# Performance work log

Measured on AMD Instinct MI355X. Metric: run time of the kernel, lower is better.

## Reference

```python
import jax, jax.numpy as jnp
import numpy as np

B, H, S, D = 4, 16, 2048, 64

def setup_inputs() -> dict:
    key = jax.random.key(0)
    kq, kk, kv = jax.random.split(key, 3)
    return {
        "query": jax.random.normal(kq, (B, H, S, D), dtype=jnp.float32),
        "key": jax.random.normal(kk, (B, H, S, D), dtype=jnp.float32),
        "value": jax.random.normal(kv, (B, H, S, D), dtype=jnp.float32),
        "dropout_p": 0,
    }

def reference(query, key, value, dropout_p):
    # qk: [B,H,S,S] materialized as in the original (unfused SDPA)
    scale = query.shape[-1] ** -0.5
    qk = jnp.einsum("bhqd,bhkd->bhqk", query, key) * scale
    attn = jax.nn.softmax(qk, axis=-1)
    # dropout_p == 0 -> identity (keeps reference deterministic)
    out = jnp.einsum("bhqk,bhkd->bhqd", attn, value)
    return out
```

## Files before the change

### kernel.cpp

```cpp
#include <hip/hip_runtime.h>
#include <hip/hip_bf16.h>

#define B_   4
#define H_   16
#define SEQ  2048
#define DH   64
#define BM   128
#define BN   128
#define NBH  (B_ * H_)
#define NELEM (NBH * SEQ * DH)

typedef __bf16 bf16x8 __attribute__((ext_vector_type(8)));
typedef float  f32x4  __attribute__((ext_vector_type(4)));
typedef unsigned short u16x8 __attribute__((ext_vector_type(8)));
typedef unsigned short u16x4 __attribute__((ext_vector_type(4)));

__device__ __forceinline__ unsigned short f2bu(float x) {
    __hip_bfloat16 h = __float2bfloat16(x);
    return __builtin_bit_cast(unsigned short, h);
}

__device__ __forceinline__ void ld_lds16(const unsigned short* g, unsigned short* l) {
    __builtin_amdgcn_global_load_lds(
        (const __attribute__((address_space(1))) unsigned int*)(g),
        (__attribute__((address_space(3))) unsigned int*)(l), 16, 0, 0);
}

__global__ __launch_bounds__(256)
void prep_kv(const float* __restrict__ K, const float* __restrict__ V,
             unsigned short* __restrict__ Kb, unsigned short* __restrict__ Vt) {
    __shared__ unsigned short tile[64 * 72];
    const int bh = blockIdx.y;
    const int s0 = blockIdx.x * 64;
    const int t  = threadIdx.x;

    {
        const float* Ki = K + (size_t)bh * SEQ * DH + (size_t)s0 * DH;
        unsigned short* Ko = Kb + (size_t)bh * SEQ * DH + (size_t)s0 * DH;
        for (int j = 0; j < 4; ++j) {
            const int e = (j * 256 + t) * 4;
            const float4 v = *reinterpret_cast<const float4*>(Ki + e);
            u16x4 u; u[0] = f2bu(v.x); u[1] = f2bu(v.y); u[2] = f2bu(v.z); u[3] = f2bu(v.w);
            *reinterpret_cast<u16x4*>(Ko + e) = u;
        }
    }

    const float* Vb = V + (size_t)bh * SEQ * DH + (size_t)s0 * DH;
    unsigned short* Vo = Vt + (size_t)bh * DH * SEQ;
    {
        const int sl = t >> 2, d0 = (t & 3) * 16;
        for (int c = 0; c < 4; ++c) {
            const float4 v = *reinterpret_cast<const float4*>(Vb + sl * DH + d0 + c * 4);
            u16x4 u; u[0] = f2bu(v.x); u[1] = f2bu(v.y); u[2] = f2bu(v.z); u[3] = f2bu(v.w);
            *reinterpret_cast<u16x4*>(&tile[sl * 72 + d0 + c * 4]) = u;
        }
    }
    __syncthreads();
    {
        const int d = t >> 2, sc = (t & 3) * 16;
        for (int j = 0; j < 4; ++j) {
            u16x4 u;
            u[0] = tile[(sc + 4 * j + 0) * 72 + d];
            u[1] = tile[(sc + 4 * j + 1) * 72 + d];
            u[2] = tile[(sc + 4 * j + 2) * 72 + d];
            u[3] = tile[(sc + 4 * j + 3) * 72 + d];
            *reinterpret_cast<u16x4*>(Vo + (size_t)d * SEQ + s0 + sc + 4 * j) = u;
        }
    }
}

__global__ __launch_bounds__(256, 3)
void fa_fwd(const float* __restrict__ Qg, const unsigned short* __restrict__ Kb,
            const unsigned short* __restrict__ Vtb, float* __restrict__ Og)
{
    __shared__ __attribute__((aligned(16))) unsigned short smem[16384];
    unsigned short* Klds = smem;
    unsigned short* Vlds = smem + 8192;

    const int tid  = threadIdx.x;
    const int lane = tid & 63;
    const int wave = tid >> 6;
    const int l15  = lane & 15;
    const int quad = lane >> 4;

    const int qtile = blockIdx.x;
    const int bh    = blockIdx.y;

    const float*          Qb  = Qg  + (size_t)bh * SEQ * DH;
    const unsigned short* Kbh = Kb  + (size_t)bh * SEQ * DH;
    const unsigned short* Vbh = Vtb + (size_t)bh * DH * SEQ;
    float*                Ob  = Og  + (size_t)bh * SEQ * DH;

    const int qrow0 = qtile * BM + wave * 32;

    const float CS = 0.125f * 1.4426950408889634f;

    bf16x8 Qf[2][2];
    for (int rt = 0; rt < 2; ++rt) {
        const float* qsrc = Qb + (size_t)(qrow0 + rt * 16 + l15) * DH + quad * 8;
        for (int kt = 0; kt < 2; ++kt) {
            const float4 a = *reinterpret_cast<const float4*>(qsrc + kt * 32);
            const float4 b = *reinterpret_cast<const float4*>(qsrc + kt * 32 + 4);
            union { bf16x8 v; unsigned short u[8]; } tmp;
            tmp.u[0] = f2bu(a.x * CS); tmp.u[1] = f2bu(a.y * CS);
            tmp.u[2] = f2bu(a.z * CS); tmp.u[3] = f2bu(a.w * CS);
            tmp.u[4] = f2bu(b.x * CS); tmp.u[5] = f2bu(b.y * CS);
            tmp.u[6] = f2bu(b.z * CS); tmp.u[7] = f2bu(b.w * CS);
            Qf[rt][kt] = tmp.v;
        }
    }

    bf16x8 ones;
    {
        union { bf16x8 v; unsigned short u[8]; } t;
        for (int i = 0; i < 8; ++i) t.u[i] = 0x3F80;
        ones = t.v;
    }
    const f32x4 fzero = {0.f, 0.f, 0.f, 0.f};

    f32x4 Oacc[2][4];
    f32x4 Lacc[2];
    for (int rt = 0; rt < 2; ++rt) {
        Lacc[rt] = fzero;
        for (int dt = 0; dt < 4; ++dt) Oacc[rt][dt] = fzero;
    }

    const unsigned short* kp[4];
    const unsigned short* vp[4];
    unsigned short* klp[4];
    unsigned short* vlp[4];
    for (int i = 0; i < 4; ++i) {
        const int beta = i * 256 + tid;
        {
            const int s    = beta >> 3;
            const int b    = beta & 7;
            const int gnat = b ^ (s & 7);
            const int grow = 32 * ((s >> 4) & 3) + 8 * ((s >> 2) & 3)
                           + 4 * (s >> 6) + (s & 3);
            kp[i]  = Kbh + (size_t)grow * DH + gnat * 8;
            klp[i] = smem + (size_t)(i * 256 + wave * 64) * 8;
        }
        {
            const int d = beta >> 4;
            const int g = (beta & 15) ^ (d & 15);
            vp[i]  = Vbh + (size_t)d * SEQ + g * 8;
            vlp[i] = smem + 8192 + (size_t)(i * 256 + wave * 64) * 8;
        }
    }

    for (int it = 0; it < SEQ / BN; ++it) {
        __syncthreads();

        for (int i = 0; i < 4; ++i) { ld_lds16(kp[i], klp[i]); kp[i] += BN * DH; }
        for (int i = 0; i < 4; ++i) { ld_lds16(vp[i], vlp[i]); vp[i] += BN; }
        __syncthreads();

        bf16x8 af[2][4];
        for (int rt = 0; rt < 2; ++rt) {
            f32x4 Sacc[8];
            for (int nt = 0; nt < 8; ++nt) {
                const int s  = nt * 16 + l15;
                const int sx = s & 7;
                const bf16x8 kf0 = *reinterpret_cast<const bf16x8*>(&Klds[s * 64 + ((quad    ) ^ sx) * 8]);
                const bf16x8 kf1 = *reinterpret_cast<const bf16x8*>(&Klds[s * 64 + ((quad + 4) ^ sx) * 8]);
                Sacc[nt] = __builtin_amdgcn_mfma_f32_16x16x32_bf16(kf0, Qf[rt][0], fzero, 0, 0, 0);
                Sacc[nt] = __builtin_amdgcn_mfma_f32_16x16x32_bf16(kf1, Qf[rt][1], Sacc[nt], 0, 0, 0);
            }
            for (int ks = 0; ks < 4; ++ks) {
                union { bf16x8 v; unsigned w[4]; } a;
                for (int h = 0; h < 2; ++h) {
                    for (int rp = 0; rp < 2; ++rp) {
                        const float p0 = __builtin_amdgcn_exp2f(Sacc[ks + 4 * h][2 * rp    ]);
                        const float p1 = __builtin_amdgcn_exp2f(Sacc[ks + 4 * h][2 * rp + 1]);
                        const unsigned u0 = __builtin_bit_cast(unsigned, p0) + 0x8000u;
                        const unsigned u1 = __builtin_bit_cast(unsigned, p1) + 0x8000u;
                        a.w[h * 2 + rp] = __builtin_amdgcn_perm(u1, u0, 0x07060302u);
                    }
                }
                af[rt][ks] = a.v;
                Lacc[rt] = __builtin_amdgcn_mfma_f32_16x16x32_bf16(a.v, ones, Lacc[rt], 0, 0, 0);
            }
        }

        for (int ks = 0; ks < 4; ++ks) {
            for (int dt = 0; dt < 4; ++dt) {
                const int d = dt * 16 + l15;
                const bf16x8 bfr = *reinterpret_cast<const bf16x8*>(
                    &Vlds[(d << 7) + (((ks * 4 + quad) ^ l15) << 3)]);
                for (int rt = 0; rt < 2; ++rt)
                    Oacc[rt][dt] = __builtin_amdgcn_mfma_f32_16x16x32_bf16(af[rt][ks], bfr, Oacc[rt][dt], 0, 0, 0);
            }
        }
    }

    for (int rt = 0; rt < 2; ++rt) {
        for (int r = 0; r < 4; ++r) {
            const float inv = 1.0f / Lacc[rt][r];
            const int row = qrow0 + rt * 16 + quad * 4 + r;
            float* orow = Ob + (size_t)row * DH + l15;
            for (int dt = 0; dt < 4; ++dt)
                orow[dt * 16] = Oacc[rt][dt][r] * inv;
        }
    }
}

extern "C" void kernel_launch(void* const* d_in, const int* in_sizes, int n_in,
                              void* d_out, int out_size, void* d_ws, size_t ws_size,
                              hipStream_t stream) {
    const float* Q = (const float*)d_in[0];
    const float* K = (const float*)d_in[1];
    const float* V = (const float*)d_in[2];
    float* O = (float*)d_out;

    unsigned short* Kb = (unsigned short*)d_ws;
    unsigned short* Vt = Kb + (size_t)NELEM;

    prep_kv<<<dim3(SEQ / 64, NBH), 256, 0, stream>>>(K, V, Kb, Vt);
    fa_fwd<<<dim3(SEQ / BM, NBH), dim3(256), 0, stream>>>(Q, Kb, Vt, O);
}
```

Baseline: 204.0 us.

## Double-buffer K/V LDS tiles, remap grid for XCD locality, add setprio

Converts the attention loop to double-buffered LDS staging so that global→LDS loads of the next K/V tile overlap MFMA work on the current tile, using one barrier per tile instead of two. Flattens the grid and remaps block IDs so that all q-tiles of a head land on the same XCD, improving L2 reuse of K/V. Adds s_setprio around MFMA phases, precomputes LDS read offsets, and widens the K conversion stores in the prep kernel. Doubling LDS lowers the occupancy hint from 3 to 2 blocks per CU.

```diff
diff --git a/kernel.cpp b/kernel.cpp
--- a/kernel.cpp
+++ b/kernel.cpp
@@ -37,11 +37,14 @@
     {
         const float* Ki = K + (size_t)bh * SEQ * DH + (size_t)s0 * DH;
         unsigned short* Ko = Kb + (size_t)bh * SEQ * DH + (size_t)s0 * DH;
-        for (int j = 0; j < 4; ++j) {
-            const int e = (j * 256 + t) * 4;
-            const float4 v = *reinterpret_cast<const float4*>(Ki + e);
-            u16x4 u; u[0] = f2bu(v.x); u[1] = f2bu(v.y); u[2] = f2bu(v.z); u[3] = f2bu(v.w);
-            *reinterpret_cast<u16x4*>(Ko + e) = u;
+        for (int jj = 0; jj < 2; ++jj) {
+            const int e = (jj * 256 + t) * 8;
+            const float4 a = *reinterpret_cast<const float4*>(Ki + e);
+            const float4 b = *reinterpret_cast<const float4*>(Ki + e + 4);
+            u16x8 u;
+            u[0] = f2bu(a.x); u[1] = f2bu(a.y); u[2] = f2bu(a.z); u[3] = f2bu(a.w);
+            u[4] = f2bu(b.x); u[5] = f2bu(b.y); u[6] = f2bu(b.z); u[7] = f2bu(b.w);
+            *reinterpret_cast<u16x8*>(Ko + e) = u;
         }
     }
 
@@ -58,24 +61,22 @@
     __syncthreads();
     {
         const int d = t >> 2, sc = (t & 3) * 16;
-        for (int j = 0; j < 4; ++j) {
+        for (int jj = 0; jj < 4; ++jj) {
             u16x4 u;
-            u[0] = tile[(sc + 4 * j + 0) * 72 + d];
-            u[1] = tile[(sc + 4 * j + 1) * 72 + d];
-            u[2] = tile[(sc + 4 * j + 2) * 72 + d];
-            u[3] = tile[(sc + 4 * j + 3) * 72 + d];
-            *reinterpret_cast<u16x4*>(Vo + (size_t)d * SEQ + s0 + sc + 4 * j) = u;
-        }
-    }
-}
-
-__global__ __launch_bounds__(256, 3)
+            u[0] = tile[(sc + 4 * jj + 0) * 72 + d];
+            u[1] = tile[(sc + 4 * jj + 1) * 72 + d];
+            u[2] = tile[(sc + 4 * jj + 2) * 72 + d];
+            u[3] = tile[(sc + 4 * jj + 3) * 72 + d];
+            *reinterpret_cast<u16x4*>(Vo + (size_t)d * SEQ + s0 + sc + 4 * jj) = u;
+        }
+    }
+}
+
+__global__ __launch_bounds__(256, 2)
 void fa_fwd(const float* __restrict__ Qg, const unsigned short* __restrict__ Kb,
             const unsigned short* __restrict__ Vtb, float* __restrict__ Og)
 {
-    __shared__ __attribute__((aligned(16))) unsigned short smem[16384];
-    unsigned short* Klds = smem;
-    unsigned short* Vlds = smem + 8192;
+    __shared__ __attribute__((aligned(16))) unsigned short smem[32768];
 
     const int tid  = threadIdx.x;
     const int lane = tid & 63;
@@ -83,8 +84,11 @@
     const int l15  = lane & 15;
     const int quad = lane >> 4;
 
-    const int qtile = blockIdx.x;
-    const int bh    = blockIdx.y;
+    const int bid   = blockIdx.x;
+    const int xcd   = bid & 7;
+    const int jj    = bid >> 3;
+    const int bh    = (xcd << 3) | (jj >> 4);
+    const int qtile = jj & 15;
 
     const float*          Qb  = Qg  + (size_t)bh * SEQ * DH;
     const unsigned short* Kbh = Kb  + (size_t)bh * SEQ * DH;
@@ -127,8 +131,7 @@
 
     const unsigned short* kp[4];
     const unsigned short* vp[4];
-    unsigned short* klp[4];
-    unsigned short* vlp[4];
+    int koff_st[4], voff_st[4];
     for (int i = 0; i < 4; ++i) {
         const int beta = i * 256 + tid;
         {
@@ -138,60 +141,116 @@
             const int grow = 32 * ((s >> 4) & 3) + 8 * ((s >> 2) & 3)
                            + 4 * (s >> 6) + (s & 3);
             kp[i]  = Kbh + (size_t)grow * DH + gnat * 8;
-            klp[i] = smem + (size_t)(i * 256 + wave * 64) * 8;
         }
         {
             const int d = beta >> 4;
             const int g = (beta & 15) ^ (d & 15);
             vp[i]  = Vbh + (size_t)d * SEQ + g * 8;
-            vlp[i] = smem + 8192 + (size_t)(i * 256 + wave * 64) * 8;
-        }
-    }
-
-    for (int it = 0; it < SEQ / BN; ++it) {
+        }
+        koff_st[i] = (i * 256 + wave * 64) * 8;
+        voff_st[i] = 8192 + (i * 256 + wave * 64) * 8;
+    }
+
+    int krd[8][2];
+#pragma unroll
+    for (int nt = 0; nt < 8; ++nt) {
+        const int s  = nt * 16 + l15;
+        const int sx = s & 7;
+        krd[nt][0] = s * 64 + ((quad    ) ^ sx) * 8;
+        krd[nt][1] = s * 64 + ((quad + 4) ^ sx) * 8;
+    }
+    int vrd[4][4];
+#pragma unroll
+    for (int ks = 0; ks < 4; ++ks)
+#pragma unroll
+        for (int dt = 0; dt < 4; ++dt) {
+            const int d = dt * 16 + l15;
+            vrd[ks][dt] = 8192 + (d << 7) + (((ks * 4 + quad) ^ l15) << 3);
+        }
+
+#define STAGE(BUF) do {                                                        \
+        _Pragma("unroll")                                                      \
+        for (int i = 0; i < 4; ++i) {                                          \
+            ld_lds16(kp[i], smem + (BUF) * 16384 + koff_st[i]);                \
+            kp[i] += BN * DH;                                                  \
+        }                                                                      \
+        _Pragma("unroll")                                                      \
+        for (int i = 0; i < 4; ++i) {                                          \
+            ld_lds16(vp[i], smem + (BUF) * 16384 + voff_st[i]);                \
+            vp[i] += BN;                                                       \
+        }                                                                      \
+    } while (0)
+
+#define COMPUTE(BUF) do {                                                      \
+        f32x4 Sacc[2][8];                                                      \
+        __builtin_amdgcn_s_setprio(1);                                         \
+        _Pragma("unroll")                                                      \
+        for (int nt = 0; nt < 8; ++nt) {                                       \
+            const bf16x8 kf0 = *reinterpret_cast<const bf16x8*>(               \
+                &smem[(BUF) * 16384 + krd[nt][0]]);                            \
+            const bf16x8 kf1 = *reinterpret_cast<const bf16x8*>(               \
+                &smem[(BUF) * 16384 + krd[nt][1]]);                            \
+            Sacc[0][nt] = __builtin_amdgcn_mfma_f32_16x16x32_bf16(kf0, Qf[0][0], fzero,       0, 0, 0); \
+            Sacc[0][nt] = __builtin_amdgcn_mfma_f32_16x16x32_bf16(kf1, Qf[0][1], Sacc[0][nt], 0, 0, 0); \
+            Sacc[1][nt] = __builtin_amdgcn_mfma_f32_16x16x32_bf16(kf0, Qf[1][0], fzero,       0, 0, 0); \
+            Sacc[1][nt] = __builtin_amdgcn_mfma_f32_16x16x32_bf16(kf1, Qf[1][1], Sacc[1][nt], 0, 0, 0); \
+        }                                                                      \
+        __builtin_amdgcn_s_setprio(0);                                         \
+        bf16x8 af[2][4];                                                       \
+        _Pragma("unroll")                                                      \
+        for (int rt = 0; rt < 2; ++rt)                                         \
+        {                                                                      \
+            _Pragma("unroll")                                                  \
+            for (int ks = 0; ks < 4; ++ks) {                                   \
+                union { bf16x8 v; unsigned w[4]; } a;                          \
+                _Pragma("unroll")                                              \
+                for (int h = 0; h < 2; ++h) {                                  \
+                    _Pragma("unroll")                                          \
+                    for (int rp = 0; rp < 2; ++rp) {                           \
+                        const float p0 = __builtin_amdgcn_exp2f(Sacc[rt][ks + 4 * h][2 * rp    ]); \
+                        const float p1 = __builtin_amdgcn_exp2f(Sacc[rt][ks + 4 * h][2 * rp + 1]); \
+                        const unsigned u0 = __builtin_bit_cast(unsigned, p0) + 0x8000u; \
+                        const unsigned u1 = __builtin_bit_cast(unsigned, p1) + 0x8000u; \
+                        a.w[h * 2 + rp] = __builtin_amdgcn_perm(u1, u0, 0x07060302u); \
+                    }                                                          \
+                }                                                              \
+                af[rt][ks] = a.v;                                              \
+                Lacc[rt] = __builtin_amdgcn_mfma_f32_16x16x32_bf16(a.v, ones, Lacc[rt], 0, 0, 0); \
+            }                                                                  \
+        }                                                                      \
+        __builtin_amdgcn_s_setprio(1);                                         \
+        _Pragma("unroll")                                                      \
+        for (int ks = 0; ks < 4; ++ks) {                                       \
+            _Pragma("unroll")                                                  \
+            for (int dt = 0; dt < 4; ++dt) {                                   \
+                const bf16x8 bfr = *reinterpret_cast<const bf16x8*>(           \
+                    &smem[(BUF) * 16384 + vrd[ks][dt]]);                       \
+                Oacc[0][dt] = __builtin_amdgcn_mfma_f32_16x16x32_bf16(af[0][ks], bfr, Oacc[0][dt], 0, 0, 0); \
+                Oacc[1][dt] = __builtin_amdgcn_mfma_f32_16x16x32_bf16(af[1][ks], bfr, Oacc[1][dt], 0, 0, 0); \
+            }                                                                  \
+        }                                                                      \
+        __builtin_amdgcn_s_setprio(0);                                         \
+    } while (0)
+
+    STAGE(0);
+    __syncthreads();
+
+#pragma unroll 1
+    for (int it2 = 0; it2 < 7; ++it2) {
+        STAGE(1);
+        COMPUTE(0);
         __syncthreads();
-
-        for (int i = 0; i < 4; ++i) { ld_lds16(kp[i], klp[i]); kp[i] += BN * DH; }
-        for (int i = 0; i < 4; ++i) { ld_lds16(vp[i], vlp[i]); vp[i] += BN; }
+        STAGE(0);
+        COMPUTE(1);
         __syncthreads();
-
-        bf16x8 af[2][4];
-        for (int rt = 0; rt < 2; ++rt) {
-            f32x4 Sacc[8];
-            for (int nt = 0; nt < 8; ++nt) {
-                const int s  = nt * 16 + l15;
-                const int sx = s & 7;
-                const bf16x8 kf0 = *reinterpret_cast<const bf16x8*>(&Klds[s * 64 + ((quad    ) ^ sx) * 8]);
-                const bf16x8 kf1 = *reinterpret_cast<const bf16x8*>(&Klds[s * 64 + ((quad + 4) ^ sx) * 8]);
-                Sacc[nt] = __builtin_amdgcn_mfma_f32_16x16x32_bf16(kf0, Qf[rt][0], fzero, 0, 0, 0);
-                Sacc[nt] = __builtin_amdgcn_mfma_f32_16x16x32_bf16(kf1, Qf[rt][1], Sacc[nt], 0, 0, 0);
-            }
-            for (int ks = 0; ks < 4; ++ks) {
-                union { bf16x8 v; unsigned w[4]; } a;
-                for (int h = 0; h < 2; ++h) {
-                    for (int rp = 0; rp < 2; ++rp) {
-                        const float p0 = __builtin_amdgcn_exp2f(Sacc[ks + 4 * h][2 * rp    ]);
-                        const float p1 = __builtin_amdgcn_exp2f(Sacc[ks + 4 * h][2 * rp + 1]);
-                        const unsigned u0 = __builtin_bit_cast(unsigned, p0) + 0x8000u;
-                        const unsigned u1 = __builtin_bit_cast(unsigned, p1) + 0x8000u;
-                        a.w[h * 2 + rp] = __builtin_amdgcn_perm(u1, u0, 0x07060302u);
-                    }
-                }
-                af[rt][ks] = a.v;
-                Lacc[rt] = __builtin_amdgcn_mfma_f32_16x16x32_bf16(a.v, ones, Lacc[rt], 0, 0, 0);
-            }
-        }
-
-        for (int ks = 0; ks < 4; ++ks) {
-            for (int dt = 0; dt < 4; ++dt) {
-                const int d = dt * 16 + l15;
-                const bf16x8 bfr = *reinterpret_cast<const bf16x8*>(
-                    &Vlds[(d << 7) + (((ks * 4 + quad) ^ l15) << 3)]);
-                for (int rt = 0; rt < 2; ++rt)
-                    Oacc[rt][dt] = __builtin_amdgcn_mfma_f32_16x16x32_bf16(af[rt][ks], bfr, Oacc[rt][dt], 0, 0, 0);
-            }
-        }
-    }
+    }
+    STAGE(1);
+    COMPUTE(0);
+    __syncthreads();
+    COMPUTE(1);
+
+#undef STAGE
+#undef COMPUTE
 
     for (int rt = 0; rt < 2; ++rt) {
         for (int r = 0; r < 4; ++r) {
@@ -216,5 +275,5 @@
     unsigned short* Vt = Kb + (size_t)NELEM;
 
     prep_kv<<<dim3(SEQ / 64, NBH), 256, 0, stream>>>(K, V, Kb, Vt);
-    fa_fwd<<<dim3(SEQ / BM, NBH), dim3(256), 0, stream>>>(Q, Kb, Vt, O);
-}
+    fa_fwd<<<dim3((SEQ / BM) * NBH), dim3(256), 0, stream>>>(Q, Kb, Vt, O);
+}
```

Result: no change. 200.7 us (-1.6%).
